# Kernel tuning notes

Measured on AMD Instinct MI355X. Metric: run time of the kernel, lower is better.

Reference implementation:

```python
import jax, jax.numpy as jnp
import numpy as np

HARMONICS = 5


def _harmonic_basis(x):
    k = jnp.arange(1, HARMONICS + 1, dtype=x.dtype)            # [H]
    kx = x[..., None] * k                                       # [B, D, H]
    sc = jnp.stack([jnp.sin(kx), jnp.cos(kx)], axis=-1)         # [B, D, H, 2]
    sc = sc.reshape(*x.shape, 2 * HARMONICS)                    # interleaved sin/cos
    ones = jnp.ones((*x.shape, 1), dtype=x.dtype)
    return jnp.concatenate([ones, sc], axis=-1)                 # [B, D, 2H+1]


def setup_inputs() -> dict:
    key = jax.random.key(0)
    k1, k2, k3 = jax.random.split(key, 3)
    B, D, F, H = 16384, 256, 11, 256
    x = jax.random.normal(k1, (B, D), dtype=jnp.float32)
    W = jax.random.normal(k2, (D, F, H), dtype=jnp.float32) * (1.0 / np.sqrt(F))
    b = jax.random.normal(k3, (D, H), dtype=jnp.float32) * 0.01
    return {"x": x, "W": W, "b": b}


def reference(x, W, b) -> jnp.ndarray:
    # basis expansion per feature, batched small GEMM, summed over features
    basis = _harmonic_basis(x)                                  # [B, D, F]
    out = jnp.einsum('bdf,dfh->bh', basis, W)                   # sum over features fused
    out = out + jnp.sum(b, axis=0)                              # sum of per-feature biases
    return out
```

## Files before the change

### kernel.cpp

```cpp
#include <hip/hip_runtime.h>
#include <hip/hip_bf16.h>


#define BDIM 16384
#define DDIM 256
#define HOUT 256
#define KTOT 2560
#define NKT  80
#define BM 64
#define BN 128

typedef __bf16 bf16x8 __attribute__((ext_vector_type(8)));
typedef float floatx4 __attribute__((ext_vector_type(4)));

__device__ __forceinline__ unsigned short f2bf(float f) {
    unsigned int u = __float_as_uint(f);
    return (unsigned short)((u + 0x7FFFu + ((u >> 16) & 1u)) >> 16);
}

__device__ __forceinline__ unsigned int pkbf(float a, float b) {
    __hip_bfloat162 r = __float22bfloat162_rn(make_float2(a, b));
    return *reinterpret_cast<unsigned int*>(&r);
}

__global__ void prep_kernel(const float* __restrict__ W, const float* __restrict__ bias,
                            unsigned short* __restrict__ Wfrag, float* __restrict__ c_part) {
    const int bid = blockIdx.x;
    const int t = threadIdx.x;
    if (bid < NKT) {
        const int kt = bid;
        const int dtile = kt / 10;
        const int f = kt - dtile * 10 + 1;
        const float* wsrc = W + ((size_t)(dtile * 32) * 11 + f) * 256 + t;
        union { unsigned short s[32]; int4 v[4]; } buf;
#pragma unroll
        for (int dd = 0; dd < 32; ++dd)
            buf.s[dd] = f2bf(wsrc[(size_t)dd * 11 * 256]);
        int4* dst = (int4*)(Wfrag + ((size_t)kt * 256 + t) * 32);
#pragma unroll
        for (int v = 0; v < 4; ++v) dst[v] = buf.v[v];
    } else {
        const int p = bid - NKT;
        float acc = 0.f;
#pragma unroll
        for (int dd = 0; dd < 32; ++dd) {
            const int d = p * 32 + dd;
            acc += W[(size_t)(d * 11) * 256 + t] + bias[(size_t)d * 256 + t];
        }
        c_part[p * 256 + t] = acc;
    }
}

__global__ __launch_bounds__(256, 2)
void kan_gemm(const float* __restrict__ x, const unsigned short* __restrict__ Wfrag,
              const float* __restrict__ c_part, float* __restrict__ out) {
    __shared__ unsigned short As[2][10 * 4 * 512];

    const int t = threadIdx.x;
    const int m0 = blockIdx.x * BM;
    const int h0 = blockIdx.y * BN;

    const int lane = t & 63;
    const int wave = t >> 6;
    const int wr = wave >> 1;
    const int wc = wave & 1;
    const int l15 = lane & 15;
    const int koff = lane >> 4;

    const int m_a = lane;
    const int q = wave;
    const int it_w = m_a >> 4;
    const int slot = (m_a & 15) + 16 * q;

    floatx4 acc[2][4];
#pragma unroll
    for (int i = 0; i < 2; ++i)
#pragma unroll
        for (int j = 0; j < 4; ++j)
            acc[i][j] = (floatx4){0.f, 0.f, 0.f, 0.f};

    const float* xrow = x + (size_t)(m0 + m_a) * DDIM;
    const unsigned short* bbase = Wfrag + (size_t)(h0 + wc * 64 + l15) * 32 + koff * 8;

    float4 xa = *(const float4*)(xrow + q * 8);
    float4 xb = *(const float4*)(xrow + q * 8 + 4);

    bf16x8 bf[5][4];
#pragma unroll
    for (int p = 0; p < 5; ++p)
#pragma unroll
        for (int j = 0; j < 4; ++j)
            bf[p][j] = *(const bf16x8*)(bbase + (size_t)p * 8192 + j * 512);

    for (int dtile = 0; dtile < 8; ++dtile) {
        unsigned short* asb = &As[dtile & 1][0];

        float xv[8] = {xa.x, xa.y, xa.z, xa.w, xb.x, xb.y, xb.z, xb.w};
        float sc[8], cc[8], sp[8], cp[8], t2c[8];
#pragma unroll
        for (int j = 0; j < 8; ++j) {
            __sincosf(xv[j], &sc[j], &cc[j]);
            t2c[j] = cc[j] + cc[j];
            sp[j] = 0.f;
            cp[j] = 1.f;
        }
#pragma unroll
        for (int k = 1; k <= 5; ++k) {
            union { unsigned int u[4]; int4 v; } vs, vc;
#pragma unroll
            for (int p = 0; p < 4; ++p) {
                vs.u[p] = pkbf(sc[2 * p], sc[2 * p + 1]);
                vc.u[p] = pkbf(cc[2 * p], cc[2 * p + 1]);
            }
            *(int4*)(&asb[((2 * k - 2) * 4 + it_w) * 512 + slot * 8]) = vs.v;
            *(int4*)(&asb[((2 * k - 1) * 4 + it_w) * 512 + slot * 8]) = vc.v;
            if (k < 5) {
#pragma unroll
                for (int j = 0; j < 8; ++j) {
                    const float ns = t2c[j] * sc[j] - sp[j];
                    const float nc = t2c[j] * cc[j] - cp[j];
                    sp[j] = sc[j]; cp[j] = cc[j];
                    sc[j] = ns;   cc[j] = nc;
                }
            }
        }
        __syncthreads();

        if (dtile < 7) {
            xa = *(const float4*)(xrow + (dtile + 1) * 32 + q * 8);
            xb = *(const float4*)(xrow + (dtile + 1) * 32 + q * 8 + 4);
        }

        bf16x8 af[3][2];
#pragma unroll
        for (int p = 0; p < 3; ++p)
#pragma unroll
            for (int i = 0; i < 2; ++i)
                af[p][i] = *(const bf16x8*)(&asb[(p * 4 + wr * 2 + i) * 512 + lane * 8]);

#pragma unroll
        for (int hs = 0; hs < 10; ++hs) {
#pragma unroll
            for (int i = 0; i < 2; ++i)
#pragma unroll
                for (int j = 0; j < 4; ++j)
                    acc[i][j] = __builtin_amdgcn_mfma_f32_16x16x32_bf16(af[hs % 3][i], bf[hs % 5][j], acc[i][j], 0, 0, 0);

            {
                int ktp = dtile * 10 + hs + 5;
                if (ktp > 79) ktp = 79;
#pragma unroll
                for (int j = 0; j < 4; ++j)
                    bf[hs % 5][j] = *(const bf16x8*)(bbase + (size_t)ktp * 8192 + j * 512);
            }
            if (hs < 7) {
#pragma unroll
                for (int i = 0; i < 2; ++i)
                    af[hs % 3][i] = *(const bf16x8*)(&asb[((hs + 3) * 4 + wr * 2 + i) * 512 + lane * 8]);
            }
        }
    }

    float cj[4];
#pragma unroll
    for (int j = 0; j < 4; ++j) {
        const int col = h0 + wc * 64 + j * 16 + l15;
        float s = 0.f;
#pragma unroll
        for (int p = 0; p < 8; ++p) s += c_part[p * 256 + col];
        cj[j] = s;
    }
#pragma unroll
    for (int i = 0; i < 2; ++i) {
        const int row0 = m0 + wr * 32 + i * 16 + koff * 4;
#pragma unroll
        for (int j = 0; j < 4; ++j) {
            const int col = h0 + wc * 64 + j * 16 + l15;
#pragma unroll
            for (int r = 0; r < 4; ++r)
                out[(size_t)(row0 + r) * HOUT + col] = acc[i][j][r] + cj[j];
        }
    }
}

extern "C" void kernel_launch(void* const* d_in, const int* in_sizes, int n_in,
                              void* d_out, int out_size, void* d_ws, size_t ws_size,
                              hipStream_t stream) {
    const float* x = (const float*)d_in[0];
    const float* W = (const float*)d_in[1];
    const float* b = (const float*)d_in[2];
    float* out = (float*)d_out;

    unsigned short* Wfrag = (unsigned short*)d_ws;
    float* c_part = (float*)((char*)d_ws + (size_t)NKT * 256 * 32 * 2);

    prep_kernel<<<NKT + 8, 256, 0, stream>>>(W, b, Wfrag, c_part);
    kan_gemm<<<dim3(BDIM / BM, HOUT / BN), 256, 0, stream>>>(x, Wfrag, c_part, out);
}
```

Baseline: 113.5 us.

## Build harmonic A-fragments in registers, dropping LDS staging and barriers

The GEMM kernel no longer writes the sin/cos basis to shared memory and reads it back. Each lane now loads the x values that match its MFMA A-fragment layout and builds the bf16 fragments directly in registers. This removes LDS traffic and the per-tile __syncthreads, but every wave sharing rows repeats the sincos/recurrence work (the two column-waves duplicate it) and register pressure rises. The prep kernel is also split into four times as many blocks for more parallelism, and the B prefetch depth drops from 5 to 4.

```diff
diff --git a/kernel.cpp b/kernel.cpp
--- a/kernel.cpp
+++ b/kernel.cpp
@@ -5,7 +5,6 @@
 #define BDIM 16384
 #define DDIM 256
 #define HOUT 256
-#define KTOT 2560
 #define NKT  80
 #define BM 64
 #define BN 128
@@ -27,20 +26,20 @@
                             unsigned short* __restrict__ Wfrag, float* __restrict__ c_part) {
     const int bid = blockIdx.x;
     const int t = threadIdx.x;
-    if (bid < NKT) {
-        const int kt = bid;
+    if (bid < 4 * NKT) {
+        const int kt = bid >> 2;
+        const int sub = bid & 3;
         const int dtile = kt / 10;
         const int f = kt - dtile * 10 + 1;
-        const float* wsrc = W + ((size_t)(dtile * 32) * 11 + f) * 256 + t;
-        union { unsigned short s[32]; int4 v[4]; } buf;
+        const int d0 = dtile * 32 + sub * 8;
+        const float* wsrc = W + ((size_t)d0 * 11 + f) * 256 + t;
+        union { unsigned short s[8]; int4 v; } buf;
 #pragma unroll
-        for (int dd = 0; dd < 32; ++dd)
+        for (int dd = 0; dd < 8; ++dd)
             buf.s[dd] = f2bf(wsrc[(size_t)dd * 11 * 256]);
-        int4* dst = (int4*)(Wfrag + ((size_t)kt * 256 + t) * 32);
-#pragma unroll
-        for (int v = 0; v < 4; ++v) dst[v] = buf.v[v];
+        *(int4*)(Wfrag + ((size_t)kt * 256 + t) * 32 + sub * 8) = buf.v;
     } else {
-        const int p = bid - NKT;
+        const int p = bid - 4 * NKT;
         float acc = 0.f;
 #pragma unroll
         for (int dd = 0; dd < 32; ++dd) {
@@ -54,8 +53,6 @@
 __global__ __launch_bounds__(256, 2)
 void kan_gemm(const float* __restrict__ x, const unsigned short* __restrict__ Wfrag,
               const float* __restrict__ c_part, float* __restrict__ out) {
-    __shared__ unsigned short As[2][10 * 4 * 512];
-
     const int t = threadIdx.x;
     const int m0 = blockIdx.x * BM;
     const int h0 = blockIdx.y * BN;
@@ -67,11 +64,6 @@
     const int l15 = lane & 15;
     const int koff = lane >> 4;
 
-    const int m_a = lane;
-    const int q = wave;
-    const int it_w = m_a >> 4;
-    const int slot = (m_a & 15) + 16 * q;
-
     floatx4 acc[2][4];
 #pragma unroll
     for (int i = 0; i < 2; ++i)
@@ -79,85 +71,83 @@
         for (int j = 0; j < 4; ++j)
             acc[i][j] = (floatx4){0.f, 0.f, 0.f, 0.f};
 
-    const float* xrow = x + (size_t)(m0 + m_a) * DDIM;
+    const float* xr0 = x + (size_t)(m0 + wr * 32 + l15) * DDIM + koff * 8;
     const unsigned short* bbase = Wfrag + (size_t)(h0 + wc * 64 + l15) * 32 + koff * 8;
 
-    float4 xa = *(const float4*)(xrow + q * 8);
-    float4 xb = *(const float4*)(xrow + q * 8 + 4);
+    float4 xc[4];
+    xc[0] = *(const float4*)(xr0 + 0);
+    xc[1] = *(const float4*)(xr0 + 4);
+    xc[2] = *(const float4*)(xr0 + 16 * DDIM + 0);
+    xc[3] = *(const float4*)(xr0 + 16 * DDIM + 4);
 
-    bf16x8 bf[5][4];
+    bf16x8 bf[4][4];
 #pragma unroll
-    for (int p = 0; p < 5; ++p)
+    for (int p = 0; p < 4; ++p)
 #pragma unroll
         for (int j = 0; j < 4; ++j)
             bf[p][j] = *(const bf16x8*)(bbase + (size_t)p * 8192 + j * 512);
 
+#pragma unroll
     for (int dtile = 0; dtile < 8; ++dtile) {
-        unsigned short* asb = &As[dtile & 1][0];
+        float4 xn[4];
+        if (dtile < 7) {
+            xn[0] = *(const float4*)(xr0 + (dtile + 1) * 32 + 0);
+            xn[1] = *(const float4*)(xr0 + (dtile + 1) * 32 + 4);
+            xn[2] = *(const float4*)(xr0 + 16 * DDIM + (dtile + 1) * 32 + 0);
+            xn[3] = *(const float4*)(xr0 + 16 * DDIM + (dtile + 1) * 32 + 4);
+        }
 
-        float xv[8] = {xa.x, xa.y, xa.z, xa.w, xb.x, xb.y, xb.z, xb.w};
-        float sc[8], cc[8], sp[8], cp[8], t2c[8];
+        float sc[16], cc[16], sp[16], cp[16], t2c[16];
 #pragma unroll
-        for (int j = 0; j < 8; ++j) {
-            __sincosf(xv[j], &sc[j], &cc[j]);
-            t2c[j] = cc[j] + cc[j];
-            sp[j] = 0.f;
-            cp[j] = 1.f;
-        }
+        for (int i = 0; i < 2; ++i)
 #pragma unroll
-        for (int k = 1; k <= 5; ++k) {
-            union { unsigned int u[4]; int4 v; } vs, vc;
+            for (int e = 0; e < 8; ++e) {
+                const int g = i * 8 + e;
+                const float xv = ((const float*)&xc[i * 2 + (e >> 2)])[e & 3];
+                __sincosf(xv, &sc[g], &cc[g]);
+                t2c[g] = cc[g] + cc[g];
+                sp[g] = 0.f;
+                cp[g] = 1.f;
+            }
+
+#pragma unroll
+        for (int hs = 0; hs < 10; ++hs) {
+            const int cur = (dtile * 10 + hs) & 3;
+            const float* src = (hs & 1) ? cc : sc;
+
+            union { unsigned int u[4]; bf16x8 v; } a0, a1;
 #pragma unroll
             for (int p = 0; p < 4; ++p) {
-                vs.u[p] = pkbf(sc[2 * p], sc[2 * p + 1]);
-                vc.u[p] = pkbf(cc[2 * p], cc[2 * p + 1]);
+                a0.u[p] = pkbf(src[2 * p], src[2 * p + 1]);
+                a1.u[p] = pkbf(src[8 + 2 * p], src[8 + 2 * p + 1]);
             }
-            *(int4*)(&asb[((2 * k - 2) * 4 + it_w) * 512 + slot * 8]) = vs.v;
-            *(int4*)(&asb[((2 * k - 1) * 4 + it_w) * 512 + slot * 8]) = vc.v;
-            if (k < 5) {
 #pragma unroll
-                for (int j = 0; j < 8; ++j) {
-                    const float ns = t2c[j] * sc[j] - sp[j];
-                    const float nc = t2c[j] * cc[j] - cp[j];
-                    sp[j] = sc[j]; cp[j] = cc[j];
-                    sc[j] = ns;   cc[j] = nc;
+            for (int j = 0; j < 4; ++j) {
+                acc[0][j] = __builtin_amdgcn_mfma_f32_16x16x32_bf16(a0.v, bf[cur][j], acc[0][j], 0, 0, 0);
+                acc[1][j] = __builtin_amdgcn_mfma_f32_16x16x32_bf16(a1.v, bf[cur][j], acc[1][j], 0, 0, 0);
+            }
+
+            {
+                int ktp = dtile * 10 + hs + 4;
+                if (ktp > 79) ktp = 79;
+#pragma unroll
+                for (int j = 0; j < 4; ++j)
+                    bf[cur][j] = *(const bf16x8*)(bbase + (size_t)ktp * 8192 + j * 512);
+            }
+
+            if ((hs & 1) && hs < 9) {
+#pragma unroll
+                for (int g = 0; g < 16; ++g) {
+                    const float ns = t2c[g] * sc[g] - sp[g];
+                    const float nc = t2c[g] * cc[g] - cp[g];
+                    sp[g] = sc[g]; cp[g] = cc[g];
+                    sc[g] = ns;   cc[g] = nc;
                 }
             }
         }
-        __syncthreads();
 
         if (dtile < 7) {
-            xa = *(const float4*)(xrow + (dtile + 1) * 32 + q * 8);
-            xb = *(const float4*)(xrow + (dtile + 1) * 32 + q * 8 + 4);
-        }
-
-        bf16x8 af[3][2];
-#pragma unroll
-        for (int p = 0; p < 3; ++p)
-#pragma unroll
-            for (int i = 0; i < 2; ++i)
-                af[p][i] = *(const bf16x8*)(&asb[(p * 4 + wr * 2 + i) * 512 + lane * 8]);
-
-#pragma unroll
-        for (int hs = 0; hs < 10; ++hs) {
-#pragma unroll
-            for (int i = 0; i < 2; ++i)
-#pragma unroll
-                for (int j = 0; j < 4; ++j)
-                    acc[i][j] = __builtin_amdgcn_mfma_f32_16x16x32_bf16(af[hs % 3][i], bf[hs % 5][j], acc[i][j], 0, 0, 0);
-
-            {
-                int ktp = dtile * 10 + hs + 5;
-                if (ktp > 79) ktp = 79;
-#pragma unroll
-                for (int j = 0; j < 4; ++j)
-                    bf[hs % 5][j] = *(const bf16x8*)(bbase + (size_t)ktp * 8192 + j * 512);
-            }
-            if (hs < 7) {
-#pragma unroll
-                for (int i = 0; i < 2; ++i)
-                    af[hs % 3][i] = *(const bf16x8*)(&asb[((hs + 3) * 4 + wr * 2 + i) * 512 + lane * 8]);
-            }
+            xc[0] = xn[0]; xc[1] = xn[1]; xc[2] = xn[2]; xc[3] = xn[3];
         }
     }
 
@@ -194,6 +184,6 @@
     unsigned short* Wfrag = (unsigned short*)d_ws;
     float* c_part = (float*)((char*)d_ws + (size_t)NKT * 256 * 32 * 2);
 
-    prep_kernel<<<NKT + 8, 256, 0, stream>>>(W, b, Wfrag, c_part);
+    prep_kernel<<<4 * NKT + 8, 256, 0, stream>>>(W, b, Wfrag, c_part);
     kan_gemm<<<dim3(BDIM / BM, HOUT / BN), 256, 0, stream>>>(x, Wfrag, c_part, out);
 }
```

After: 122.9 us. +8.3%, slower.
